# Optimization experiments

Measured on AMD Instinct MI355X. Metric: run time of the kernel, lower is better.

## Reference

```python
import jax, jax.numpy as jnp
import numpy as np

EMB_W, COMMIT_W, ENT_W = 1.0, 0.25, 0.1  # loss weights from init_kwargs


def setup_inputs() -> dict:
    key = jax.random.key(0)
    k1, k2 = jax.random.split(key)
    B, H, W, D, K = 32, 32, 32, 64, 1024
    inputs = jax.random.normal(k1, (B, H, W, D), dtype=jnp.float32)
    # keras RandomUniform default: U(-0.05, 0.05)
    codebook = jax.random.uniform(k2, (K, D), dtype=jnp.float32, minval=-0.05, maxval=0.05)
    return {"inputs": inputs, "codebook": codebook}


def reference(inputs, codebook):
    # inputs: [B,H,W,D], codebook: [K,D]
    D = inputs.shape[-1]
    x = inputs.reshape(-1, D)  # [N,D]
    dist = (
        jnp.sum(x * x, axis=-1, keepdims=True)
        - 2.0 * (x @ codebook.T)
        + jnp.sum(codebook * codebook, axis=-1)
    )  # [N,K]
    tokens = jnp.argmin(dist, axis=-1)  # [N]
    emb = codebook[tokens].reshape(inputs.shape)  # [B,H,W,D]

    embedding_loss = EMB_W * jnp.mean((jax.lax.stop_gradient(emb) - inputs) ** 2)
    commitment_loss = COMMIT_W * jnp.mean((emb - jax.lax.stop_gradient(inputs)) ** 2)
    # 'entropy' loss as written in call(): mean over codebook of per-code min distance
    entropy_loss = ENT_W * jnp.mean(jnp.min(dist, axis=0))
    loss = embedding_loss + commitment_loss + entropy_loss

    # training=True path: straight-through estimator
    out = inputs + jax.lax.stop_gradient(emb - inputs)
    return out, loss
```

## Files before the change

kernel.cpp:

```cpp
#include <hip/hip_runtime.h>
#include <math.h>

#define NROWS 32768
#define NCODE 1024
#define AMB_CAP 8192
#define GAP_THRESH 1.5e-4f

typedef __attribute__((ext_vector_type(8))) short bf16x8;
typedef __attribute__((ext_vector_type(4))) float f32x4;

__device__ __forceinline__ unsigned short bf16_rne(float f) {
    unsigned u = __float_as_uint(f);
    unsigned r = u + 0x7FFFu + ((u >> 16) & 1u);
    return (unsigned short)(r >> 16);
}

__global__ __launch_bounds__(64) void vq_prep(
    const float* __restrict__ cb, float* __restrict__ cn4,
    unsigned* __restrict__ minK, unsigned* __restrict__ counter,
    float* __restrict__ gsumsq, unsigned* __restrict__ ticket,
    unsigned short* __restrict__ wsB)
{
    int c = blockIdx.x * 64 + threadIdx.x;
    if (c == 0) { *counter = 0u; *gsumsq = 0.f; *ticket = 0u; }
    float v[64];
    const float4* src = (const float4*)(cb + (size_t)c * 64);
    float s = 0.f;
    #pragma unroll
    for (int i = 0; i < 16; i++) {
        float4 t = src[i];
        v[i*4+0] = t.x; v[i*4+1] = t.y; v[i*4+2] = t.z; v[i*4+3] = t.w;
        s += t.x*t.x + t.y*t.y + t.z*t.z + t.w*t.w;
    }
    cn4[c] = s + 4.0f;
    minK[c] = 0x7F800000u;
    int cc = c >> 6, ct = (c >> 4) & 3, cl = c & 15;
    #pragma unroll
    for (int q = 0; q < 4; q++) {
        int half = q & 1, lo = q >> 1;
        #pragma unroll
        for (int g = 0; g < 4; g++) {
            unsigned short u8[8] __attribute__((aligned(16)));
            #pragma unroll
            for (int j = 0; j < 8; j++) {
                float f = -2.0f * v[half*32 + g*8 + j];
                unsigned short h = bf16_rne(f);
                if (lo) h = bf16_rne(f - __uint_as_float((unsigned)h << 16));
                u8[j] = h;
            }
            size_t off = (size_t)cc * 8192 + ct * 2048 + q * 512 + (g * 16 + cl) * 8;
            *(uint4*)(wsB + off) = *(const uint4*)u8;
        }
    }
}

__global__ __launch_bounds__(512, 4) void vq_main(
    const float* __restrict__ x, const float* __restrict__ cb,
    const unsigned short* __restrict__ wsB, const float* __restrict__ cn4,
    float* __restrict__ out, unsigned* __restrict__ minK,
    unsigned* __restrict__ counter, int* __restrict__ amb,
    float* __restrict__ gsumsq)
{
    __shared__ float    cn4L[1024];
    __shared__ unsigned scrE[1024];
    __shared__ float mD1[128], mD2[128];
    __shared__ int   mI1[128];
    __shared__ int   tokS[64];
    __shared__ float redS[8];

    const int tid = threadIdx.x;
    const int lane = tid & 63;
    const int wi = tid >> 6;
    const int g = wi >> 1;
    const int h = wi & 1;
    const int ln15 = lane & 15;
    const int q = lane >> 4;
    const int row0 = blockIdx.x * 64;

    cn4L[tid]       = cn4[tid];
    cn4L[512 + tid] = cn4[512 + tid];
    scrE[tid]       = 0x7F800000u;
    scrE[512 + tid] = 0x7F800000u;

    bf16x8 Ah0, Ah1, Al0, Al1;
    float xnm4[4];
    {
        const float* xr = x + (size_t)(row0 + g*16 + ln15) * 64 + q * 8;
        float4 f0 = *(const float4*)xr;
        float4 f1 = *(const float4*)(xr + 4);
        float4 f2 = *(const float4*)(xr + 32);
        float4 f3 = *(const float4*)(xr + 36);
        float fa[8] = {f0.x,f0.y,f0.z,f0.w,f1.x,f1.y,f1.z,f1.w};
        float fb[8] = {f2.x,f2.y,f2.z,f2.w,f3.x,f3.y,f3.z,f3.w};
        unsigned short hh8[8] __attribute__((aligned(16)));
        unsigned short ll8[8] __attribute__((aligned(16)));
        unsigned short h28[8] __attribute__((aligned(16)));
        unsigned short l28[8] __attribute__((aligned(16)));
        float ss = 0.f;
        #pragma unroll
        for (int j = 0; j < 8; j++) {
            ss += fa[j]*fa[j] + fb[j]*fb[j];
            unsigned short hh = bf16_rne(fa[j]);
            hh8[j] = hh; ll8[j] = bf16_rne(fa[j] - __uint_as_float((unsigned)hh << 16));
            hh = bf16_rne(fb[j]);
            h28[j] = hh; l28[j] = bf16_rne(fb[j] - __uint_as_float((unsigned)hh << 16));
        }
        Ah0 = *(const bf16x8*)hh8; Al0 = *(const bf16x8*)ll8;
        Ah1 = *(const bf16x8*)h28; Al1 = *(const bf16x8*)l28;
        ss += __shfl_xor(ss, 16);
        ss += __shfl_xor(ss, 32);
        #pragma unroll
        for (int r = 0; r < 4; r++)
            xnm4[r] = __shfl(ss, (q << 2) | r, 64) - 4.0f;
    }
    __syncthreads();

    float d1[4], d2[4];
    int   i1[4];
    #pragma unroll
    for (int r = 0; r < 4; r++) { d1[r] = INFINITY; d2[r] = INFINITY; i1[r] = 0; }

    const char* wsQ = (const char*)wsB + (size_t)h * 131072 + lane * 16;
    #pragma unroll 4
    for (int t = 0; t < 32; t++) {
        const char* tb = wsQ + t * 4096;
        bf16x8 Bh0 = *(const bf16x8*)(tb);
        bf16x8 Bh1 = *(const bf16x8*)(tb + 1024);
        bf16x8 Bl0 = *(const bf16x8*)(tb + 2048);
        bf16x8 Bl1 = *(const bf16x8*)(tb + 3072);
        const int kid = h*512 + t*16 + ln15;
        const float cn4v = cn4L[kid];
        f32x4 a0 = {cn4v, cn4v, cn4v, cn4v};
        a0 = __builtin_amdgcn_mfma_f32_16x16x32_bf16(Ah0, Bh0, a0, 0, 0, 0);
        a0 = __builtin_amdgcn_mfma_f32_16x16x32_bf16(Ah1, Bh1, a0, 0, 0, 0);
        a0 = __builtin_amdgcn_mfma_f32_16x16x32_bf16(Ah0, Bl0, a0, 0, 0, 0);
        a0 = __builtin_amdgcn_mfma_f32_16x16x32_bf16(Ah1, Bl1, a0, 0, 0, 0);
        a0 = __builtin_amdgcn_mfma_f32_16x16x32_bf16(Al0, Bh0, a0, 0, 0, 0);
        a0 = __builtin_amdgcn_mfma_f32_16x16x32_bf16(Al1, Bh1, a0, 0, 0, 0);
        float cm = INFINITY;
        #pragma unroll
        for (int r = 0; r < 4; r++) {
            float wv = a0[r];
            d2[r] = fminf(fmaxf(wv, d1[r]), d2[r]);
            bool lt = wv < d1[r];
            i1[r] = lt ? kid : i1[r];
            d1[r] = fminf(wv, d1[r]);
            cm = fminf(cm, wv + xnm4[r]);
        }
        atomicMin(&scrE[kid], __float_as_uint(cm));
    }

    #pragma unroll
    for (int d = 1; d < 16; d <<= 1) {
        #pragma unroll
        for (int r = 0; r < 4; r++) {
            float od1 = __shfl_xor(d1[r], d);
            int   oi1 = __shfl_xor(i1[r], d);
            float od2 = __shfl_xor(d2[r], d);
            bool take = (od1 < d1[r]) || (od1 == d1[r] && oi1 < i1[r]);
            float loser = take ? d1[r] : od1;
            d2[r] = fminf(fminf(d2[r], od2), loser);
            d1[r] = take ? od1 : d1[r];
            i1[r] = take ? oi1 : i1[r];
        }
    }
    if (ln15 == 0) {
        #pragma unroll
        for (int r = 0; r < 4; r++) {
            int idx = (g*16 + q*4 + r) * 2 + h;
            mD1[idx] = d1[r]; mI1[idx] = i1[r]; mD2[idx] = d2[r];
        }
    }
    __syncthreads();

    if (tid < 64) {
        float a1 = mD1[tid*2],   b1 = mD1[tid*2+1];
        int   ai = mI1[tid*2],   bi = mI1[tid*2+1];
        float a2 = mD2[tid*2],   b2 = mD2[tid*2+1];
        bool ta = (a1 < b1) || (a1 == b1 && ai < bi);
        float D1 = ta ? a1 : b1;
        int   I1 = ta ? ai : bi;
        float D2 = ta ? fminf(a2, b1) : fminf(b2, a1);
        tokS[tid] = I1;
        if (D2 - D1 < GAP_THRESH) {
            unsigned idx = atomicAdd(counter, 1u);
            if (idx < AMB_CAP) { amb[2*idx] = row0 + tid; amb[2*idx+1] = I1; }
        }
    }

    {
        unsigned u0 = scrE[tid];
        if (u0 < minK[tid]) atomicMin(&minK[tid], u0);
        unsigned u1 = scrE[512 + tid];
        if (u1 < minK[512 + tid]) atomicMin(&minK[512 + tid], u1);
    }
    __syncthreads();

    {
        float acc2 = 0.f;
        #pragma unroll
        for (int uu = 0; uu < 2; uu++) {
            int u = uu*512 + tid;
            int row = u >> 4, c4 = u & 15;
            int tok = tokS[row];
            float4 c = ((const float4*)(cb + (size_t)tok*64))[c4];
            float4 xx = ((const float4*)(x + (size_t)(row0 + row)*64))[c4];
            ((float4*)(out + (size_t)(row0 + row)*64))[c4] = c;
            float dx = c.x-xx.x, dy = c.y-xx.y, dz = c.z-xx.z, dw = c.w-xx.w;
            acc2 += dx*dx + dy*dy + dz*dz + dw*dw;
        }
        #pragma unroll
        for (int o = 32; o > 0; o >>= 1) acc2 += __shfl_down(acc2, o);
        if (lane == 0) redS[wi] = acc2;
        __syncthreads();
        if (tid == 0) {
            float t = 0.f;
            #pragma unroll
            for (int w = 0; w < 8; w++) t += redS[w];
            atomicAdd(gsumsq, t);
        }
    }
}

__global__ __launch_bounds__(256) void vq_tail(
    const float* __restrict__ x, const float* __restrict__ cb,
    float* __restrict__ out, const unsigned* __restrict__ counter,
    const int* __restrict__ amb, float* __restrict__ gsumsq,
    unsigned* __restrict__ ticket, const unsigned* __restrict__ minK,
    float* __restrict__ out_loss)
{
    __shared__ __align__(16) float cbS[16384];
    __shared__ double xs[64];
    __shared__ double bd[256];
    __shared__ int    bi[256];
    __shared__ unsigned lastS;
    __shared__ float redS[4];

    const int tid = threadIdx.x;

    unsigned cnt = *counter; if (cnt > AMB_CAP) cnt = AMB_CAP;
    for (unsigned i = blockIdx.x; i < cnt; i += gridDim.x) {
        int row = amb[2*i], oldk = amb[2*i+1];
        __syncthreads();
        if (tid < 64) xs[tid] = (double)x[(size_t)row*64 + tid];
        __syncthreads();
        double xn = 0.0;
        #pragma unroll 8
        for (int d = 0; d < 64; d++) xn += xs[d]*xs[d];
        double best = INFINITY; int bk = 1 << 30;
        for (int b = 0; b < 4; b++) {
            __syncthreads();
            #pragma unroll
            for (int k = 0; k < 16; k++)
                ((float4*)cbS)[k*256 + tid] = ((const float4*)cb)[b*4096 + k*256 + tid];
            __syncthreads();
            int kcode = b*256 + tid;
            const int t6 = tid & 63;
            double dot = 0.0, cn2 = 0.0;
            #pragma unroll 8
            for (int dd = 0; dd < 64; dd++) {
                int d = (dd + t6) & 63;
                double cv = (double)cbS[tid*64 + d];
                dot = fma(xs[d], cv, dot);
                cn2 = fma(cv, cv, cn2);
            }
            double dist = (xn - 2.0*dot) + cn2;
            if (dist < best || (dist == best && kcode < bk)) { best = dist; bk = kcode; }
        }
        bd[tid] = best; bi[tid] = bk;
        __syncthreads();
        for (int s = 128; s > 0; s >>= 1) {
            if (tid < s) {
                double od = bd[tid+s]; int ok = bi[tid+s];
                if (od < bd[tid] || (od == bd[tid] && ok < bi[tid])) { bd[tid] = od; bi[tid] = ok; }
            }
            __syncthreads();
        }
        int bestk = bi[0];
        if (bestk != oldk) {
            double part = 0.0;
            if (tid < 64) {
                float cn = cb[(size_t)bestk*64 + tid];
                float co = cb[(size_t)oldk*64 + tid];
                out[(size_t)row*64 + tid] = cn;
                double dn = (double)cn - xs[tid];
                double dl = (double)co - xs[tid];
                part = dn*dn - dl*dl;
            }
            __syncthreads();
            bd[tid] = part;
            __syncthreads();
            for (int s = 128; s > 0; s >>= 1) {
                if (tid < s) bd[tid] += bd[tid+s];
                __syncthreads();
            }
            if (tid == 0) atomicAdd(gsumsq, (float)bd[0]);
        }
    }

    __syncthreads();
    if (tid == 0) {
        __threadfence();
        lastS = (atomicAdd(ticket, 1u) == 63u) ? 1u : 0u;
    }
    __syncthreads();
    if (lastS) {
        __threadfence();
        float s = 0.f;
        #pragma unroll
        for (int jj = 0; jj < 4; jj++)
            s += __uint_as_float(minK[jj*256 + tid]);
        #pragma unroll
        for (int o = 32; o > 0; o >>= 1) s += __shfl_down(s, o);
        if ((tid & 63) == 0) redS[tid >> 6] = s;
        __syncthreads();
        if (tid == 0) {
            float gs = atomicAdd(gsumsq, 0.0f);
            float tot = redS[0] + redS[1] + redS[2] + redS[3];
            out_loss[0] = 1.25f * (gs / 2097152.0f) + 0.1f * (tot / 1024.0f);
        }
    }
}

extern "C" void kernel_launch(void* const* d_in, const int* in_sizes, int n_in,
                              void* d_out, int out_size, void* d_ws, size_t ws_size,
                              hipStream_t stream) {
    const float* x  = (const float*)d_in[0];
    const float* cb = (const float*)d_in[1];
    float* out = (float*)d_out;

    char* ws = (char*)d_ws;
    unsigned*       counter = (unsigned*)ws;
    float*          gsumsq  = (float*)(ws + 4);
    unsigned*       ticket  = (unsigned*)(ws + 8);
    float*          cn4     = (float*)(ws + 1024);
    unsigned*       minK    = (unsigned*)(ws + 8192);
    int*            amb     = (int*)(ws + 16384);
    unsigned short* wsB     = (unsigned short*)(ws + 131072);

    vq_prep<<<16,  64,  0, stream>>>(cb, cn4, minK, counter, gsumsq, ticket, wsB);
    vq_main<<<512, 512, 0, stream>>>(x, cb, wsB, cn4, out, minK, counter, amb, gsumsq);
    vq_tail<<<64,  256, 0, stream>>>(x, cb, out, counter, amb, gsumsq, ticket, minK,
                                     out + 2097152);
}
```

Baseline: 114.9 us.

## Fuse ambiguity-resolution tail into main kernel via grid-wide spin barrier

```diff
diff --git a/kernel.cpp b/kernel.cpp
--- a/kernel.cpp
+++ b/kernel.cpp
@@ -19,10 +19,10 @@
     const float* __restrict__ cb, float* __restrict__ cn4,
     unsigned* __restrict__ minK, unsigned* __restrict__ counter,
     float* __restrict__ gsumsq, unsigned* __restrict__ ticket,
-    unsigned short* __restrict__ wsB)
+    unsigned* __restrict__ ticket2, unsigned short* __restrict__ wsB)
 {
     int c = blockIdx.x * 64 + threadIdx.x;
-    if (c == 0) { *counter = 0u; *gsumsq = 0.f; *ticket = 0u; }
+    if (c == 0) { *counter = 0u; *gsumsq = 0.f; *ticket = 0u; *ticket2 = 0u; }
     float v[64];
     const float4* src = (const float4*)(cb + (size_t)c * 64);
     float s = 0.f;
@@ -54,19 +54,32 @@
     }
 }
 
+struct MainS {
+    float    cn4L[1024];
+    unsigned scrE[1024];
+    float    mD1[128], mD2[128];
+    int      mI1[128];
+    int      tokS[64];
+    float    redS[8];
+};
+struct TailS {
+    float    cbS[16384];
+    double   xs[64];
+    double   bd[256];
+    int      bi[256];
+    unsigned lastS;
+    float    redS2[8];
+};
+
 __global__ __launch_bounds__(512, 4) void vq_main(
     const float* __restrict__ x, const float* __restrict__ cb,
     const unsigned short* __restrict__ wsB, const float* __restrict__ cn4,
     float* __restrict__ out, unsigned* __restrict__ minK,
     unsigned* __restrict__ counter, int* __restrict__ amb,
-    float* __restrict__ gsumsq)
+    float* __restrict__ gsumsq, unsigned* __restrict__ ticket,
+    unsigned* __restrict__ ticket2, float* __restrict__ out_loss)
 {
-    __shared__ float    cn4L[1024];
-    __shared__ unsigned scrE[1024];
-    __shared__ float mD1[128], mD2[128];
-    __shared__ int   mI1[128];
-    __shared__ int   tokS[64];
-    __shared__ float redS[8];
+    __shared__ __align__(16) union { MainS m; TailS t; } S;
 
     const int tid = threadIdx.x;
     const int lane = tid & 63;
@@ -77,10 +90,10 @@
     const int q = lane >> 4;
     const int row0 = blockIdx.x * 64;
 
-    cn4L[tid]       = cn4[tid];
-    cn4L[512 + tid] = cn4[512 + tid];
-    scrE[tid]       = 0x7F800000u;
-    scrE[512 + tid] = 0x7F800000u;
+    S.m.cn4L[tid]       = cn4[tid];
+    S.m.cn4L[512 + tid] = cn4[512 + tid];
+    S.m.scrE[tid]       = 0x7F800000u;
+    S.m.scrE[512 + tid] = 0x7F800000u;
 
     bf16x8 Ah0, Ah1, Al0, Al1;
     float xnm4[4];
@@ -129,7 +142,7 @@
         bf16x8 Bl0 = *(const bf16x8*)(tb + 2048);
         bf16x8 Bl1 = *(const bf16x8*)(tb + 3072);
         const int kid = h*512 + t*16 + ln15;
-        const float cn4v = cn4L[kid];
+        const float cn4v = S.m.cn4L[kid];
         f32x4 a0 = {cn4v, cn4v, cn4v, cn4v};
         a0 = __builtin_amdgcn_mfma_f32_16x16x32_bf16(Ah0, Bh0, a0, 0, 0, 0);
         a0 = __builtin_amdgcn_mfma_f32_16x16x32_bf16(Ah1, Bh1, a0, 0, 0, 0);
@@ -147,7 +160,7 @@
             d1[r] = fminf(wv, d1[r]);
             cm = fminf(cm, wv + xnm4[r]);
         }
-        atomicMin(&scrE[kid], __float_as_uint(cm));
+        atomicMin(&S.m.scrE[kid], __float_as_uint(cm));
     }
 
     #pragma unroll
@@ -168,20 +181,20 @@
         #pragma unroll
         for (int r = 0; r < 4; r++) {
             int idx = (g*16 + q*4 + r) * 2 + h;
-            mD1[idx] = d1[r]; mI1[idx] = i1[r]; mD2[idx] = d2[r];
+            S.m.mD1[idx] = d1[r]; S.m.mI1[idx] = i1[r]; S.m.mD2[idx] = d2[r];
         }
     }
     __syncthreads();
 
     if (tid < 64) {
-        float a1 = mD1[tid*2],   b1 = mD1[tid*2+1];
-        int   ai = mI1[tid*2],   bi = mI1[tid*2+1];
-        float a2 = mD2[tid*2],   b2 = mD2[tid*2+1];
+        float a1 = S.m.mD1[tid*2],   b1 = S.m.mD1[tid*2+1];
+        int   ai = S.m.mI1[tid*2],   bi = S.m.mI1[tid*2+1];
+        float a2 = S.m.mD2[tid*2],   b2 = S.m.mD2[tid*2+1];
         bool ta = (a1 < b1) || (a1 == b1 && ai < bi);
         float D1 = ta ? a1 : b1;
         int   I1 = ta ? ai : bi;
         float D2 = ta ? fminf(a2, b1) : fminf(b2, a1);
-        tokS[tid] = I1;
+        S.m.tokS[tid] = I1;
         if (D2 - D1 < GAP_THRESH) {
             unsigned idx = atomicAdd(counter, 1u);
             if (idx < AMB_CAP) { amb[2*idx] = row0 + tid; amb[2*idx+1] = I1; }
@@ -189,9 +202,9 @@
     }
 
     {
-        unsigned u0 = scrE[tid];
+        unsigned u0 = S.m.scrE[tid];
         if (u0 < minK[tid]) atomicMin(&minK[tid], u0);
-        unsigned u1 = scrE[512 + tid];
+        unsigned u1 = S.m.scrE[512 + tid];
         if (u1 < minK[512 + tid]) atomicMin(&minK[512 + tid], u1);
     }
     __syncthreads();
@@ -202,7 +215,7 @@
         for (int uu = 0; uu < 2; uu++) {
             int u = uu*512 + tid;
             int row = u >> 4, c4 = u & 15;
-            int tok = tokS[row];
+            int tok = S.m.tokS[row];
             float4 c = ((const float4*)(cb + (size_t)tok*64))[c4];
             float4 xx = ((const float4*)(x + (size_t)(row0 + row)*64))[c4];
             ((float4*)(out + (size_t)(row0 + row)*64))[c4] = c;
@@ -211,112 +224,114 @@
         }
         #pragma unroll
         for (int o = 32; o > 0; o >>= 1) acc2 += __shfl_down(acc2, o);
-        if (lane == 0) redS[wi] = acc2;
+        if (lane == 0) S.m.redS[wi] = acc2;
         __syncthreads();
         if (tid == 0) {
             float t = 0.f;
             #pragma unroll
-            for (int w = 0; w < 8; w++) t += redS[w];
+            for (int w = 0; w < 8; w++) t += S.m.redS[w];
             atomicAdd(gsumsq, t);
         }
     }
-}
-
-__global__ __launch_bounds__(256) void vq_tail(
-    const float* __restrict__ x, const float* __restrict__ cb,
-    float* __restrict__ out, const unsigned* __restrict__ counter,
-    const int* __restrict__ amb, float* __restrict__ gsumsq,
-    unsigned* __restrict__ ticket, const unsigned* __restrict__ minK,
-    float* __restrict__ out_loss)
-{
-    __shared__ __align__(16) float cbS[16384];
-    __shared__ double xs[64];
-    __shared__ double bd[256];
-    __shared__ int    bi[256];
-    __shared__ unsigned lastS;
-    __shared__ float redS[4];
-
-    const int tid = threadIdx.x;
+
+    __syncthreads();
+    __threadfence();
+    if (tid == 0) atomicAdd(ticket2, 1u);
+    if (blockIdx.x >= 64) return;
+
+    if (tid == 0) {
+        while (atomicAdd(ticket2, 0u) < 512u) __builtin_amdgcn_s_sleep(8);
+    }
+    __syncthreads();
+    __threadfence();
 
     unsigned cnt = *counter; if (cnt > AMB_CAP) cnt = AMB_CAP;
-    for (unsigned i = blockIdx.x; i < cnt; i += gridDim.x) {
+    for (unsigned i = blockIdx.x; i < cnt; i += 64u) {
         int row = amb[2*i], oldk = amb[2*i+1];
         __syncthreads();
-        if (tid < 64) xs[tid] = (double)x[(size_t)row*64 + tid];
+        if (tid < 64) S.t.xs[tid] = (double)x[(size_t)row*64 + tid];
         __syncthreads();
         double xn = 0.0;
         #pragma unroll 8
-        for (int d = 0; d < 64; d++) xn += xs[d]*xs[d];
+        for (int d = 0; d < 64; d++) xn += S.t.xs[d]*S.t.xs[d];
         double best = INFINITY; int bk = 1 << 30;
         for (int b = 0; b < 4; b++) {
             __syncthreads();
             #pragma unroll
-            for (int k = 0; k < 16; k++)
-                ((float4*)cbS)[k*256 + tid] = ((const float4*)cb)[b*4096 + k*256 + tid];
-            __syncthreads();
-            int kcode = b*256 + tid;
-            const int t6 = tid & 63;
-            double dot = 0.0, cn2 = 0.0;
-            #pragma unroll 8
-            for (int dd = 0; dd < 64; dd++) {
-                int d = (dd + t6) & 63;
-                double cv = (double)cbS[tid*64 + d];
-                dot = fma(xs[d], cv, dot);
-                cn2 = fma(cv, cv, cn2);
-            }
-            double dist = (xn - 2.0*dot) + cn2;
-            if (dist < best || (dist == best && kcode < bk)) { best = dist; bk = kcode; }
-        }
-        bd[tid] = best; bi[tid] = bk;
+            for (int k = 0; k < 8; k++)
+                ((float4*)S.t.cbS)[k*512 + tid] = ((const float4*)cb)[b*4096 + k*512 + tid];
+            __syncthreads();
+            if (tid < 256) {
+                int kcode = b*256 + tid;
+                const int t6 = tid & 63;
+                double dot = 0.0, cn2 = 0.0;
+                #pragma unroll 8
+                for (int dd = 0; dd < 64; dd++) {
+                    int d = (dd + t6) & 63;
+                    double cv = (double)S.t.cbS[tid*64 + d];
+                    dot = fma(S.t.xs[d], cv, dot);
+                    cn2 = fma(cv, cv, cn2);
+                }
+                double dist = (xn - 2.0*dot) + cn2;
+                if (dist < best || (dist == best && kcode < bk)) { best = dist; bk = kcode; }
+            }
+        }
+        if (tid < 256) { S.t.bd[tid] = best; S.t.bi[tid] = bk; }
         __syncthreads();
         for (int s = 128; s > 0; s >>= 1) {
             if (tid < s) {
-                double od = bd[tid+s]; int ok = bi[tid+s];
-                if (od < bd[tid] || (od == bd[tid] && ok < bi[tid])) { bd[tid] = od; bi[tid] = ok; }
-            }
-            __syncthreads();
-        }
-        int bestk = bi[0];
+                double od = S.t.bd[tid+s]; int ok = S.t.bi[tid+s];
+                if (od < S.t.bd[tid] || (od == S.t.bd[tid] && ok < S.t.bi[tid])) {
+                    S.t.bd[tid] = od; S.t.bi[tid] = ok;
+                }
+            }
+            __syncthreads();
+        }
+        int bestk = S.t.bi[0];
         if (bestk != oldk) {
             double part = 0.0;
             if (tid < 64) {
                 float cn = cb[(size_t)bestk*64 + tid];
                 float co = cb[(size_t)oldk*64 + tid];
                 out[(size_t)row*64 + tid] = cn;
-                double dn = (double)cn - xs[tid];
-                double dl = (double)co - xs[tid];
+                double dn = (double)cn - S.t.xs[tid];
+                double dl = (double)co - S.t.xs[tid];
                 part = dn*dn - dl*dl;
             }
             __syncthreads();
-            bd[tid] = part;
+            if (tid < 256) S.t.bd[tid] = part;
             __syncthreads();
             for (int s = 128; s > 0; s >>= 1) {
-                if (tid < s) bd[tid] += bd[tid+s];
+                if (tid < s) S.t.bd[tid] += S.t.bd[tid+s];
                 __syncthreads();
             }
-            if (tid == 0) atomicAdd(gsumsq, (float)bd[0]);
+            if (tid == 0) atomicAdd(gsumsq, (float)S.t.bd[0]);
         }
     }
 
     __syncthreads();
     if (tid == 0) {
         __threadfence();
-        lastS = (atomicAdd(ticket, 1u) == 63u) ? 1u : 0u;
-    }
-    __syncthreads();
-    if (lastS) {
+        S.t.lastS = (atomicAdd(ticket, 1u) == 63u) ? 1u : 0u;
+    }
+    __syncthreads();
+    if (S.t.lastS) {
         __threadfence();
         float s = 0.f;
-        #pragma unroll
-        for (int jj = 0; jj < 4; jj++)
-            s += __uint_as_float(minK[jj*256 + tid]);
+        if (tid < 256) {
+            #pragma unroll
+            for (int jj = 0; jj < 4; jj++)
+                s += __uint_as_float(minK[jj*256 + tid]);
+        }
         #pragma unroll
         for (int o = 32; o > 0; o >>= 1) s += __shfl_down(s, o);
-        if ((tid & 63) == 0) redS[tid >> 6] = s;
+        if (lane == 0) S.t.redS2[wi] = s;
         __syncthreads();
         if (tid == 0) {
             float gs = atomicAdd(gsumsq, 0.0f);
-            float tot = redS[0] + redS[1] + redS[2] + redS[3];
+            float tot = 0.f;
+            #pragma unroll
+            for (int w = 0; w < 8; w++) tot += S.t.redS2[w];
             out_loss[0] = 1.25f * (gs / 2097152.0f) + 0.1f * (tot / 1024.0f);
         }
     }
@@ -333,13 +348,13 @@
     unsigned*       counter = (unsigned*)ws;
     float*          gsumsq  = (float*)(ws + 4);
     unsigned*       ticket  = (unsigned*)(ws + 8);
+    unsigned*       ticket2 = (unsigned*)(ws + 12);
     float*          cn4     = (float*)(ws + 1024);
     unsigned*       minK    = (unsigned*)(ws + 8192);
     int*            amb     = (int*)(ws + 16384);
     unsigned short* wsB     = (unsigned short*)(ws + 131072);
 
-    vq_prep<<<16,  64,  0, stream>>>(cb, cn4, minK, counter, gsumsq, ticket, wsB);
-    vq_main<<<512, 512, 0, stream>>>(x, cb, wsB, cn4, out, minK, counter, amb, gsumsq);
-    vq_tail<<<64,  256, 0, stream>>>(x, cb, out, counter, amb, gsumsq, ticket, minK,
-                                     out + 2097152);
+    vq_prep<<<16,  64,  0, stream>>>(cb, cn4, minK, counter, gsumsq, ticket, ticket2, wsB);
+    vq_main<<<512, 512, 0, stream>>>(x, cb, wsB, cn4, out, minK, counter, amb, gsumsq,
+                                     ticket, ticket2, out + 2097152);
 }
```

After: 209.3 us. 1.82x slower.
